# Performance work log

Measured on AMD Instinct MI355X. Metric: run time of the kernel, lower is better.

The kernel has to match this reference:

```python
import jax, jax.numpy as jnp
import numpy as np

SIZES = [4096, 12288, 20480, 20480, 8192]  # atoms of degree 0..4 (atoms sorted by degree)
N_ATOMS = sum(SIZES)
BATCH = 1024
N_TASKS, N_CLASSES = 12, 2
BN_EPS = 1e-3  # keras BatchNormalization default epsilon


def setup_inputs() -> dict:
    key = jax.random.key(0)
    ks = jax.random.split(key, 20)
    inp = {}
    inp["atom_features"] = jax.random.normal(ks[0], (N_ATOMS, 75), jnp.float32)
    starts = np.concatenate([[0], np.cumsum(SIZES)[:-1]])
    inp["degree_slice"] = jnp.asarray(np.stack([starts, np.array(SIZES)], 1), jnp.int32)
    inp["membership"] = jax.random.randint(ks[1], (N_ATOMS,), 0, BATCH, jnp.int32)
    inp["n_samples"] = BATCH
    for d in range(1, 5):
        inp[f"deg_adj_{d}"] = jax.random.randint(ks[1 + d], (SIZES[d], d), 0, N_ATOMS, jnp.int32)

    def w(k, shape, s=0.05):
        return s * jax.random.normal(k, shape, jnp.float32)

    # GraphConv weights: order [relW_deg1, selfW_deg1, ..., relW_deg4, selfW_deg4, selfW_deg0]
    inp["gc1_W"] = w(ks[6], (9, 75, 256)); inp["gc1_b"] = w(ks[7], (9, 256))
    inp["gc2_W"] = w(ks[8], (9, 256, 256)); inp["gc2_b"] = w(ks[9], (9, 256))

    def bn_params(k, c):  # rows: gamma, beta, moving_mean, moving_var
        g = 1.0 + 0.1 * jax.random.normal(k, (c,), jnp.float32)
        b = 0.1 * jax.random.normal(jax.random.fold_in(k, 1), (c,), jnp.float32)
        return jnp.stack([g, b, jnp.zeros((c,), jnp.float32), jnp.ones((c,), jnp.float32)])

    inp["bn1"] = bn_params(ks[10], 256)
    inp["bn2"] = bn_params(ks[11], 256)
    inp["bn3"] = bn_params(ks[12], 512)
    inp["dense_W"] = w(ks[13], (256, 512)); inp["dense_b"] = w(ks[14], (512,))
    inp["head_W"] = w(ks[15], (2 * 512, N_TASKS * N_CLASSES)); inp["head_b"] = w(ks[16], (N_TASKS * N_CLASSES,))
    return inp


def _graph_conv(x, adjs, W, b):
    # degree-0 atoms: self transform only (last weight matrix)
    pieces = [x[: SIZES[0]] @ W[8] + b[8]]
    off = SIZES[0]
    for d in range(1, 5):
        nd = SIZES[d]
        self_atoms = x[off: off + nd]
        rel = jnp.take(x, adjs[d - 1], axis=0).sum(axis=1)  # [nd, F] neighbor sum
        out = rel @ W[2 * (d - 1)] + b[2 * (d - 1)] + self_atoms @ W[2 * d - 1] + b[2 * d - 1]
        pieces.append(out)
        off += nd
    return jax.nn.relu(jnp.concatenate(pieces, axis=0))


def _graph_pool(x, adjs):
    pieces = [x[: SIZES[0]]]  # degree-0: passthrough
    off = SIZES[0]
    for d in range(1, 5):
        nd = SIZES[d]
        self_atoms = x[off: off + nd]
        neigh = jnp.take(x, adjs[d - 1], axis=0)  # [nd, d, F]
        pieces.append(jnp.maximum(self_atoms, neigh.max(axis=1)))
        off += nd
    return jnp.concatenate(pieces, axis=0)


def _bn(x, p):  # inference batchnorm with moving stats
    g, b, m, v = p
    return g * (x - m) * jax.lax.rsqrt(v + BN_EPS) + b


def reference(atom_features, degree_slice, membership, n_samples,
              deg_adj_1, deg_adj_2, deg_adj_3, deg_adj_4,
              gc1_W, gc1_b, gc2_W, gc2_b, bn1, bn2, bn3,
              dense_W, dense_b, head_W, head_b):
    adjs = (deg_adj_1, deg_adj_2, deg_adj_3, deg_adj_4)
    x = atom_features
    for W, b, bn in ((gc1_W, gc1_b, bn1), (gc2_W, gc2_b, bn2)):
        x = _bn(_graph_conv(x, adjs, W, b), bn)
        x = _graph_pool(x, adjs)
    h = _bn(jax.nn.relu(x @ dense_W + dense_b), bn3)  # [N_ATOMS, 512]
    # GraphGather: per-molecule sum and max, tanh activation
    seg_sum = jax.ops.segment_sum(h, membership, num_segments=BATCH)
    seg_max = jax.ops.segment_max(h, membership, num_segments=BATCH)
    fp = jnp.tanh(jnp.concatenate([seg_sum, seg_max], axis=1))  # neural fingerprint [BATCH, 1024]
    logits = (fp @ head_W + head_b).reshape(BATCH, N_TASKS, N_CLASSES)[: int(n_samples)]  # trim
    return jax.nn.softmax(logits, axis=-1), logits, fp
```

## Files before the change

kernel.cpp:

```cpp
#include <hip/hip_runtime.h>
#include <hip/hip_bf16.h>
#include <math.h>

#define NA 65536
#define MAXSEG 160

typedef _Float16 half8 __attribute__((ext_vector_type(8)));
typedef _Float16 h4    __attribute__((ext_vector_type(4)));
typedef float float4v  __attribute__((ext_vector_type(4)));


__device__ __forceinline__ int unperm128(int p) {
    return (p & ~127) + (((p & 127) & 7) << 4) + ((p & 127) >> 3);
}

__device__ __forceinline__ void atom_seg(int atom, int& d, int& loc,
                                         const int* a1, const int* a2,
                                         const int* a3, const int* a4,
                                         const int*& adj) {
    if (atom < 4096)       { d = 0; loc = 0; adj = nullptr; }
    else if (atom < 16384) { d = 1; adj = a1; loc = atom - 4096; }
    else if (atom < 36864) { d = 2; adj = a2; loc = atom - 16384; }
    else if (atom < 57344) { d = 3; adj = a3; loc = atom - 36864; }
    else                   { d = 4; adj = a4; loc = atom - 57344; }
}

__global__ void zero_count_kernel(int* __restrict__ count) {
    int i = blockIdx.x * 256 + threadIdx.x;
    if (i < 1024) count[i] = 0;
}

__global__ void bucket_kernel(const int* __restrict__ mem, int* __restrict__ count,
                              int* __restrict__ list) {
    int i = blockIdx.x * 256 + threadIdx.x;
    int seg = mem[i];
    int pos = atomicAdd(&count[seg], 1);
    if (pos < MAXSEG) list[seg * MAXSEG + pos] = i;
}

__global__ void cvt_w1_kernel(const float* __restrict__ gc1W, const float* __restrict__ gc1b,
                              _Float16* __restrict__ Wc1, float* __restrict__ bias1) {
    int idx = blockIdx.x * 256 + threadIdx.x;
    if (idx < 204800) {
        int k = idx % 160, n = (idx / 160) & 255, seg = idx / (160 * 256);
        float v = 0.f;
        if (k < 75) { int w = (seg == 0) ? 8 : (2 * seg - 1); v = gc1W[(w * 75 + k) * 256 + n]; }
        else if (k < 150 && seg > 0) { int w = 2 * (seg - 1); v = gc1W[(w * 75 + (k - 75)) * 256 + n]; }
        Wc1[(size_t)(seg * 256 + n) * 160 + k] = (_Float16)v;
    }
    if (idx < 1280) {
        int n = idx & 255, seg = idx >> 8;
        bias1[idx] = (seg == 0) ? gc1b[8 * 256 + n]
                                : gc1b[(2 * seg - 1) * 256 + n] + gc1b[2 * (seg - 1) * 256 + n];
    }
}

__global__ void cvt_w2_kernel(const float* __restrict__ gc2W, const float* __restrict__ gc2b,
                              _Float16* __restrict__ Wc2, float* __restrict__ bias2) {
    int idx = blockIdx.x * 256 + threadIdx.x;
    if (idx < 655360) {
        int k = idx & 511, n = (idx >> 9) & 255, seg = idx >> 17;
        float v = 0.f;
        if (k < 256) {
            int w = (seg == 0) ? 8 : (2 * seg - 1);
            int chan = unperm128(k);
            v = gc2W[(w * 256 + chan) * 256 + n];
        } else if (seg > 0) {
            int w = 2 * (seg - 1);
            int chan = unperm128(k - 256);
            v = gc2W[(w * 256 + chan) * 256 + n];
        }
        Wc2[(size_t)(seg * 256 + n) * 512 + k] = (_Float16)v;
    }
    if (idx < 1280) {
        int n = idx & 255, seg = idx >> 8;
        bias2[idx] = (seg == 0) ? gc2b[8 * 256 + n]
                                : gc2b[(2 * seg - 1) * 256 + n] + gc2b[2 * (seg - 1) * 256 + n];
    }
}

__global__ void cvt_wd_kernel(const float* __restrict__ dW, _Float16* __restrict__ dWt) {
    int idx = blockIdx.x * 256 + threadIdx.x;
    int n = idx >> 8, k = idx & 255;
    dWt[(size_t)n * 256 + k] = (_Float16)dW[(size_t)unperm128(k) * 512 + n];
}

__global__ void cvt_hw_kernel(const float* __restrict__ hW, float* __restrict__ hWt) {
    int idx = blockIdx.x * 256 + threadIdx.x;
    int o = idx / 1024, k = idx & 1023;
    hWt[idx] = hW[k * 24 + o];
}

__global__ __launch_bounds__(256) void gather1_kernel(
    const float* __restrict__ af,
    const int* __restrict__ a1, const int* __restrict__ a2,
    const int* __restrict__ a3, const int* __restrict__ a4,
    _Float16* __restrict__ X1) {
    int atom = blockIdx.x * 4 + (threadIdx.x >> 6);
    int lane = threadIdx.x & 63;
    int d, loc; const int* adj;
    atom_seg(atom, d, loc, a1, a2, a3, a4, adj);
    int nb[4];
    for (int j = 0; j < d; j++) nb[j] = adj[(size_t)loc * d + j];
    for (int k = lane; k < 75; k += 64) {
        X1[(size_t)atom * 160 + k] = (_Float16)af[(size_t)atom * 75 + k];
        float s = 0.f;
        for (int j = 0; j < d; j++) s += af[(size_t)nb[j] * 75 + k];
        X1[(size_t)atom * 160 + 75 + k] = (_Float16)s;
    }
    if (lane < 10) X1[(size_t)atom * 160 + 150 + lane] = (_Float16)0.f;
}

__global__ __launch_bounds__(256) void gather2n_kernel(
    const _Float16* __restrict__ p,
    const int* __restrict__ a1, const int* __restrict__ a2,
    const int* __restrict__ a3, const int* __restrict__ a4,
    _Float16* __restrict__ Xn) {
    int atom = blockIdx.x * 4 + (threadIdx.x >> 6);
    int lane = threadIdx.x & 63;
    int d, loc; const int* adj;
    atom_seg(atom, d, loc, a1, a2, a3, a4, adj);
    int nb[4];
    for (int j = 0; j < d; j++) nb[j] = adj[(size_t)loc * d + j];
    float s0 = 0.f, s1 = 0.f, s2 = 0.f, s3 = 0.f;
    for (int j = 0; j < d; j++) {
        h4 v = *(const h4*)(p + (size_t)nb[j] * 256 + lane * 4);
        s0 += (float)v[0]; s1 += (float)v[1]; s2 += (float)v[2]; s3 += (float)v[3];
    }
    h4 o; o[0] = (_Float16)s0; o[1] = (_Float16)s1; o[2] = (_Float16)s2; o[3] = (_Float16)s3;
    *(h4*)(Xn + (size_t)atom * 256 + lane * 4) = o;
}

template<int K, int N, int BK, int SPLIT>
__global__ __launch_bounds__(256) void gemm_kernel(
    const _Float16* __restrict__ X, const _Float16* __restrict__ Xn,
    const _Float16* __restrict__ Wt,
    const float* __restrict__ bias, const float* __restrict__ bnp,
    int wstride, int bstride, _Float16* __restrict__ out) {
    constexpr int NC8 = BK / 8;
    __shared__ _Float16 As[128 * BK];
    __shared__ _Float16 Bs[128 * BK];
    constexpr int nb = N / 128;
    int G = gridDim.x;
    int bid = (blockIdx.x & 7) * (G >> 3) + (blockIdx.x >> 3);
    int m0 = (bid / nb) * 128, n0 = (bid % nb) * 128;
    int t = m0 >> 7;
    int seg = (t < 32) ? 0 : (t < 128) ? 1 : (t < 288) ? 2 : (t < 448) ? 3 : 4;
    const _Float16* Wb = Wt + (size_t)seg * wstride;
    const float* bia = bias + seg * bstride;
    int tid = threadIdx.x, lane = tid & 63, wave = tid >> 6;
    int wm = wave * 32;
    int lrow = lane & 15, lq = lane >> 4;
    float4v acc[2][8] = {};
    for (int kc = 0; kc < K / BK; kc++) {
        #pragma unroll
        for (int p = tid; p < 128 * NC8; p += 256) {
            int row = p / NC8, c8 = p % NC8;
            int cs = c8 ^ (row & (NC8 - 1));
            const _Float16* srcA;
            if (!SPLIT) {
                srcA = X + (size_t)(m0 + row) * K + kc * BK + c8 * 8;
            } else {
                int kcol = kc * BK + c8 * 8;
                srcA = (kcol < 256) ? X  + (size_t)(m0 + row) * 256 + kcol
                                    : Xn + (size_t)(m0 + row) * 256 + (kcol - 256);
            }
            *(uint4*)(As + row * BK + cs * 8) = *(const uint4*)srcA;
            *(uint4*)(Bs + row * BK + cs * 8) =
                *(const uint4*)(Wb + (size_t)(n0 + row) * K + kc * BK + c8 * 8);
        }
        __syncthreads();
        #pragma unroll
        for (int kl = 0; kl < BK / 32; kl++) {
            half8 af[2], bf[8];
            #pragma unroll
            for (int i = 0; i < 2; i++) {
                int ra = wm + i * 16 + lrow;
                int ca = (kl * 4 + lq) ^ (ra & (NC8 - 1));
                af[i] = *(const half8*)(As + ra * BK + ca * 8);
            }
            #pragma unroll
            for (int j = 0; j < 8; j++) {
                int rb = j * 16 + lrow;
                int cb = (kl * 4 + lq) ^ (rb & (NC8 - 1));
                bf[j] = *(const half8*)(Bs + rb * BK + cb * 8);
            }
            #pragma unroll
            for (int mi = 0; mi < 2; mi++)
                #pragma unroll
                for (int ni = 0; ni < 8; ni++)
                    acc[mi][ni] = __builtin_amdgcn_mfma_f32_16x16x32_f16(af[mi], bf[ni], acc[mi][ni], 0, 0, 0);
        }
        __syncthreads();
    }
    float bv[8], sc[8], mn[8], be[8];
    #pragma unroll
    for (int ni = 0; ni < 8; ni++) {
        int c = n0 + ni * 16 + lrow;
        bv[ni] = bia[c];
        float g = bnp[c], vr = bnp[3 * N + c];
        mn[ni] = bnp[2 * N + c]; be[ni] = bnp[N + c];
        sc[ni] = g * rsqrtf(vr + 1e-3f);
    }
    #pragma unroll
    for (int mi = 0; mi < 2; mi++) {
        #pragma unroll
        for (int r = 0; r < 4; r++) {
            half8 pack;
            #pragma unroll
            for (int ni = 0; ni < 8; ni++) {
                float v = acc[mi][ni][r] + bv[ni];
                v = fmaxf(v, 0.f);
                v = sc[ni] * (v - mn[ni]) + be[ni];
                pack[ni] = (_Float16)v;
            }
            int row = m0 + wm + mi * 16 + lq * 4 + r;
            *(half8*)(out + (size_t)row * N + n0 + lrow * 8) = pack;
        }
    }
}

__global__ __launch_bounds__(256) void pool_f16_kernel(
    const _Float16* __restrict__ x,
    const int* __restrict__ a1, const int* __restrict__ a2,
    const int* __restrict__ a3, const int* __restrict__ a4,
    _Float16* __restrict__ out) {
    int atom = blockIdx.x * 4 + (threadIdx.x >> 6);
    int lane = threadIdx.x & 63;
    int d, loc; const int* adj;
    atom_seg(atom, d, loc, a1, a2, a3, a4, adj);
    h4 m = *(const h4*)(x + (size_t)atom * 256 + lane * 4);
    float m0 = (float)m[0], m1 = (float)m[1], m2 = (float)m[2], m3 = (float)m[3];
    for (int j = 0; j < d; j++) {
        int nb = adj[(size_t)loc * d + j];
        h4 v = *(const h4*)(x + (size_t)nb * 256 + lane * 4);
        m0 = fmaxf(m0, (float)v[0]); m1 = fmaxf(m1, (float)v[1]);
        m2 = fmaxf(m2, (float)v[2]); m3 = fmaxf(m3, (float)v[3]);
    }
    h4 o; o[0] = (_Float16)m0; o[1] = (_Float16)m1; o[2] = (_Float16)m2; o[3] = (_Float16)m3;
    *(h4*)(out + (size_t)atom * 256 + lane * 4) = o;
}

__global__ __launch_bounds__(512) void seg_reduce_kernel(
    const _Float16* __restrict__ h, const int* __restrict__ count,
    const int* __restrict__ list, float* __restrict__ fp) {
    int seg = blockIdx.x, c = threadIdx.x;
    int chan = unperm128(c);
    int n = count[seg]; if (n > MAXSEG) n = MAXSEG;
    float sum = 0.f, mx = -INFINITY;
    for (int a = 0; a < n; a++) {
        int row = list[seg * MAXSEG + a];
        float v = (float)h[(size_t)row * 512 + c];
        sum += v; mx = fmaxf(mx, v);
    }
    fp[(size_t)seg * 1024 + chan] = tanhf(sum);
    fp[(size_t)seg * 1024 + 512 + chan] = tanhf(mx);
}

__global__ __launch_bounds__(256) void head_kernel(
    const float* __restrict__ fp, const float* __restrict__ hWt,
    const float* __restrict__ hb, float* __restrict__ logits,
    float* __restrict__ probs) {
    __shared__ float fps[1024];
    __shared__ float red[32];
    int s = blockIdx.x;
    for (int i = threadIdx.x; i < 1024; i += 256) fps[i] = fp[(size_t)s * 1024 + i];
    __syncthreads();
    int t = threadIdx.x;
    int o = t >> 3, kp = t & 7;
    float acc = 0.f;
    if (o < 24) {
        const float* w = hWt + (size_t)o * 1024 + kp * 128;
        const float* f = fps + kp * 128;
        #pragma unroll 8
        for (int i = 0; i < 128; i++) acc = fmaf(f[i], w[i], acc);
    }
    acc += __shfl_down(acc, 4, 64);
    acc += __shfl_down(acc, 2, 64);
    acc += __shfl_down(acc, 1, 64);
    if (o < 24 && kp == 0) red[o] = acc + hb[o];
    __syncthreads();
    if (t < 24) {
        float a = red[t];
        float an = red[t ^ 1];
        logits[(size_t)s * 24 + t] = a;
        probs[(size_t)s * 24 + t] = 1.f / (1.f + expf(an - a));
    }
}

extern "C" void kernel_launch(void* const* d_in, const int* in_sizes, int n_in,
                              void* d_out, int out_size, void* d_ws, size_t ws_size,
                              hipStream_t stream) {
    const float* af         = (const float*)d_in[0];
    const int*   membership = (const int*)d_in[2];
    const int*   a1 = (const int*)d_in[4];
    const int*   a2 = (const int*)d_in[5];
    const int*   a3 = (const int*)d_in[6];
    const int*   a4 = (const int*)d_in[7];
    const float* gc1W = (const float*)d_in[8];
    const float* gc1b = (const float*)d_in[9];
    const float* gc2W = (const float*)d_in[10];
    const float* gc2b = (const float*)d_in[11];
    const float* bn1  = (const float*)d_in[12];
    const float* bn2  = (const float*)d_in[13];
    const float* bn3  = (const float*)d_in[14];
    const float* dW   = (const float*)d_in[15];
    const float* db   = (const float*)d_in[16];
    const float* hW   = (const float*)d_in[17];
    const float* hb   = (const float*)d_in[18];

    float* out    = (float*)d_out;
    float* probs  = out;
    float* logits = out + 24576;
    float* fp     = out + 49152;

    _Float16* Wc1  = (_Float16*)d_ws;
    _Float16* Wc2  = Wc1 + 204800;
    _Float16* dWt  = Wc2 + 655360;
    float* bias1   = (float*)(dWt + 131072);
    float* bias2   = bias1 + 1280;
    float* hWt     = bias2 + 1280;
    int* count     = (int*)(hWt + 24576);
    int* list      = count + 1024;
    _Float16* bufBig = (_Float16*)(list + 163840);
    _Float16* bufY   = bufBig + (size_t)NA * 512;
    _Float16* bufP   = bufY + (size_t)NA * 256;
    _Float16* X1 = bufBig;
    _Float16* Xn = bufBig + (size_t)NA * 256;
    _Float16* h  = bufBig;

    zero_count_kernel<<<4, 256, 0, stream>>>(count);
    bucket_kernel<<<256, 256, 0, stream>>>(membership, count, list);
    cvt_w1_kernel<<<800, 256, 0, stream>>>(gc1W, gc1b, Wc1, bias1);
    cvt_w2_kernel<<<2560, 256, 0, stream>>>(gc2W, gc2b, Wc2, bias2);
    cvt_wd_kernel<<<512, 256, 0, stream>>>(dW, dWt);
    cvt_hw_kernel<<<96, 256, 0, stream>>>(hW, hWt);

    gather1_kernel<<<16384, 256, 0, stream>>>(af, a1, a2, a3, a4, X1);
    gemm_kernel<160, 256, 32, 0><<<1024, 256, 0, stream>>>(X1, nullptr, Wc1, bias1, bn1,
                                                           256 * 160, 256, bufY);
    pool_f16_kernel<<<16384, 256, 0, stream>>>(bufY, a1, a2, a3, a4, bufP);
    gather2n_kernel<<<16384, 256, 0, stream>>>(bufP, a1, a2, a3, a4, Xn);
    gemm_kernel<512, 256, 64, 1><<<1024, 256, 0, stream>>>(bufP, Xn, Wc2, bias2, bn2,
                                                           256 * 512, 256, bufY);
    pool_f16_kernel<<<16384, 256, 0, stream>>>(bufY, a1, a2, a3, a4, bufP);
    gemm_kernel<256, 512, 64, 0><<<2048, 256, 0, stream>>>(bufP, nullptr, dWt, db, bn3,
                                                           0, 0, h);
    seg_reduce_kernel<<<1024, 512, 0, stream>>>(h, count, list, fp);
    head_kernel<<<1024, 256, 0, stream>>>(fp, hWt, hb, logits, probs);
}
```

Measured before the change: 364.2 us.

## Use direct global-to-LDS async loads and 2x2 wave tiling in GEMM

The GEMM tile loader now uses global_load_lds to write 16-byte chunks straight into shared memory instead of staging them through registers. The swizzle is inverted so each lane's fixed LDS slot maps to the correct global source. Waves are rearranged from 4x1 (32x128 each) to a 2x2 grid (64x64 each), which balances A and B fragment loads from LDS. The output column permutation changes to match, so downstream consumers must agree with the new channel ordering. Pipelining is unchanged: still a single buffer with two barriers per K step.

```diff
diff --git a/kernel.cpp b/kernel.cpp
--- a/kernel.cpp
+++ b/kernel.cpp
@@ -8,6 +8,13 @@
 typedef _Float16 half8 __attribute__((ext_vector_type(8)));
 typedef _Float16 h4    __attribute__((ext_vector_type(4)));
 typedef float float4v  __attribute__((ext_vector_type(4)));
+
+typedef __attribute__((address_space(3))) unsigned int lds_uint;
+typedef __attribute__((address_space(1))) const unsigned int g_uint;
+
+__device__ __forceinline__ void async16(const void* g, void* l) {
+    __builtin_amdgcn_global_load_lds((g_uint*)g, (lds_uint*)l, 16, 0, 0);
+}
 
 
 __device__ __forceinline__ int unperm128(int p) {
@@ -63,12 +70,10 @@
         float v = 0.f;
         if (k < 256) {
             int w = (seg == 0) ? 8 : (2 * seg - 1);
-            int chan = unperm128(k);
-            v = gc2W[(w * 256 + chan) * 256 + n];
+            v = gc2W[(w * 256 + unperm128(k)) * 256 + n];
         } else if (seg > 0) {
             int w = 2 * (seg - 1);
-            int chan = unperm128(k - 256);
-            v = gc2W[(w * 256 + chan) * 256 + n];
+            v = gc2W[(w * 256 + unperm128(k - 256)) * 256 + n];
         }
         Wc2[(size_t)(seg * 256 + n) * 512 + k] = (_Float16)v;
     }
@@ -138,8 +143,9 @@
     const float* __restrict__ bias, const float* __restrict__ bnp,
     int wstride, int bstride, _Float16* __restrict__ out) {
     constexpr int NC8 = BK / 8;
-    __shared__ _Float16 As[128 * BK];
-    __shared__ _Float16 Bs[128 * BK];
+    constexpr int MASK = NC8 - 1;
+    __shared__ __align__(16) _Float16 As[128 * BK];
+    __shared__ __align__(16) _Float16 Bs[128 * BK];
     constexpr int nb = N / 128;
     int G = gridDim.x;
     int bid = (blockIdx.x & 7) * (G >> 3) + (blockIdx.x >> 3);
@@ -149,73 +155,73 @@
     const _Float16* Wb = Wt + (size_t)seg * wstride;
     const float* bia = bias + seg * bstride;
     int tid = threadIdx.x, lane = tid & 63, wave = tid >> 6;
-    int wm = wave * 32;
+    int wm = (wave >> 1) * 64, wn = (wave & 1) * 64;
     int lrow = lane & 15, lq = lane >> 4;
-    float4v acc[2][8] = {};
+    float4v acc[4][4] = {};
     for (int kc = 0; kc < K / BK; kc++) {
         #pragma unroll
-        for (int p = tid; p < 128 * NC8; p += 256) {
-            int row = p / NC8, c8 = p % NC8;
-            int cs = c8 ^ (row & (NC8 - 1));
-            const _Float16* srcA;
+        for (int q = 0; q < NC8 / 2; q++) {
+            int slot = q * 256 + wave * 64 + lane;
+            int row = slot / NC8;
+            int cs = slot & MASK;
+            int c8 = cs ^ (row & MASK);
+            const _Float16* gA;
             if (!SPLIT) {
-                srcA = X + (size_t)(m0 + row) * K + kc * BK + c8 * 8;
+                gA = X + (size_t)(m0 + row) * K + kc * BK + c8 * 8;
             } else {
                 int kcol = kc * BK + c8 * 8;
-                srcA = (kcol < 256) ? X  + (size_t)(m0 + row) * 256 + kcol
-                                    : Xn + (size_t)(m0 + row) * 256 + (kcol - 256);
+                gA = (kcol < 256) ? X  + (size_t)(m0 + row) * 256 + kcol
+                                  : Xn + (size_t)(m0 + row) * 256 + (kcol - 256);
             }
-            *(uint4*)(As + row * BK + cs * 8) = *(const uint4*)srcA;
-            *(uint4*)(Bs + row * BK + cs * 8) =
-                *(const uint4*)(Wb + (size_t)(n0 + row) * K + kc * BK + c8 * 8);
+            async16(gA, As + (size_t)(q * 256 + wave * 64) * 8);
+            const _Float16* gB = Wb + (size_t)(n0 + row) * K + kc * BK + c8 * 8;
+            async16(gB, Bs + (size_t)(q * 256 + wave * 64) * 8);
         }
         __syncthreads();
         #pragma unroll
         for (int kl = 0; kl < BK / 32; kl++) {
-            half8 af[2], bf[8];
+            half8 af[4], bf[4];
             #pragma unroll
-            for (int i = 0; i < 2; i++) {
+            for (int i = 0; i < 4; i++) {
                 int ra = wm + i * 16 + lrow;
-                int ca = (kl * 4 + lq) ^ (ra & (NC8 - 1));
+                int ca = (kl * 4 + lq) ^ (ra & MASK);
                 af[i] = *(const half8*)(As + ra * BK + ca * 8);
+                int rb = wn + i * 16 + lrow;
+                int cb = (kl * 4 + lq) ^ (rb & MASK);
+                bf[i] = *(const half8*)(Bs + rb * BK + cb * 8);
             }
             #pragma unroll
-            for (int j = 0; j < 8; j++) {
-                int rb = j * 16 + lrow;
-                int cb = (kl * 4 + lq) ^ (rb & (NC8 - 1));
-                bf[j] = *(const half8*)(Bs + rb * BK + cb * 8);
-            }
-            #pragma unroll
-            for (int mi = 0; mi < 2; mi++)
+            for (int mi = 0; mi < 4; mi++)
                 #pragma unroll
-                for (int ni = 0; ni < 8; ni++)
+                for (int ni = 0; ni < 4; ni++)
                     acc[mi][ni] = __builtin_amdgcn_mfma_f32_16x16x32_f16(af[mi], bf[ni], acc[mi][ni], 0, 0, 0);
         }
         __syncthreads();
     }
-    float bv[8], sc[8], mn[8], be[8];
+    float bv[4], sc[4], mn[4], be[4];
     #pragma unroll
-    for (int ni = 0; ni < 8; ni++) {
-        int c = n0 + ni * 16 + lrow;
+    for (int ni = 0; ni < 4; ni++) {
+        int c = n0 + wn + ni * 16 + lrow;
         bv[ni] = bia[c];
         float g = bnp[c], vr = bnp[3 * N + c];
         mn[ni] = bnp[2 * N + c]; be[ni] = bnp[N + c];
         sc[ni] = g * rsqrtf(vr + 1e-3f);
     }
+    int p0 = n0 + lrow * 8 + (wave & 1) * 4;
     #pragma unroll
-    for (int mi = 0; mi < 2; mi++) {
+    for (int mi = 0; mi < 4; mi++) {
         #pragma unroll
         for (int r = 0; r < 4; r++) {
-            half8 pack;
+            h4 pack;
             #pragma unroll
-            for (int ni = 0; ni < 8; ni++) {
+            for (int ni = 0; ni < 4; ni++) {
                 float v = acc[mi][ni][r] + bv[ni];
                 v = fmaxf(v, 0.f);
                 v = sc[ni] * (v - mn[ni]) + be[ni];
                 pack[ni] = (_Float16)v;
             }
             int row = m0 + wm + mi * 16 + lq * 4 + r;
-            *(half8*)(out + (size_t)row * N + n0 + lrow * 8) = pack;
+            *(h4*)(out + (size_t)row * N + p0) = pack;
         }
     }
 }
```

Result: faster. 348.3 us (-4.4%).
